# Optimization experiments

Hardware: AMD Instinct MI355X
Metric: run time of the kernel (lower is better)

The kernel has to match this reference:

```python
import jax, jax.numpy as jnp
import numpy as np

C = 128          # hidden_channels
H = 2            # num_heads
D = C // H       # head dim
L = 2            # HGTConv layers
T = 3            # node types: 0=paper, 1=author, 2=venue
N_NODES = [300000, 200000, 5000]
# edge types: (src_type_idx, dst_type_idx, n_edges)
EDGE_TYPES = [(1, 0, 150000), (0, 1, 150000), (0, 0, 120000),
              (0, 0, 120000), (0, 2, 30000), (2, 0, 30000)]
R = len(EDGE_TYPES)
N_LABEL = 200000
OFFS = np.concatenate([[0], np.cumsum(N_NODES)])  # global node offsets
N_TOT = int(OFFS[-1])


def setup_inputs() -> dict:
    key = jax.random.key(0)
    ks = iter(jax.random.split(key, 64))
    nrm = lambda shape: jax.random.normal(next(ks), shape, jnp.float32) * 0.05
    inp = {
        'paper_idx': jnp.arange(N_NODES[0]),
        'author_idx': jnp.arange(N_NODES[1]),
        'venue_idx': jnp.arange(N_NODES[2]),
    }
    for r, (s, d, e) in enumerate(EDGE_TYPES):
        inp[f'src{r}'] = jax.random.randint(next(ks), (e,), 0, N_NODES[s])
        inp[f'dst{r}'] = jax.random.randint(next(ks), (e,), 0, N_NODES[d])
    inp['edge_label_index'] = jax.random.randint(next(ks), (2, N_LABEL), 0, N_NODES[0])
    # learned parameters
    inp['paper_emb'] = nrm((N_NODES[0], C))
    inp['author_emb'] = nrm((N_NODES[1], C))
    inp['venue_emb'] = nrm((N_NODES[2], C))
    inp['lin_w'] = nrm((T, C, C));  inp['lin_b'] = nrm((T, C))           # HGT.lin_dict
    inp['kqv_w'] = nrm((L, T, C, 3 * C));  inp['kqv_b'] = nrm((L, T, 3 * C))
    inp['krel_w'] = nrm((L, R, H, D, D));  inp['vrel_w'] = nrm((L, R, H, D, D))
    inp['prel'] = jnp.ones((L, R, H), jnp.float32)                       # p_rel prior
    inp['out_w'] = nrm((L, T, C, C));  inp['out_b'] = nrm((L, T, C))     # out_lin
    inp['skip'] = jnp.ones((L, T), jnp.float32)                          # skip gate
    return inp


def _hgt_layer(xs, kqv_w, kqv_b, krel_w, vrel_w, prel, out_w, out_b, skip, srcs, dsts):
    # xs: list of [Nt, C] node features per node type
    k_d, q_d, v_d = [], [], []
    for t in range(T):
        kqv = xs[t] @ kqv_w[t] + kqv_b[t]                 # [Nt, 3C]
        k, q, v = jnp.split(kqv, 3, axis=1)
        k_d.append(k.reshape(-1, H, D))
        q_d.append(q.reshape(-1, H, D))
        v_d.append(v.reshape(-1, H, D))
    logits, vals, dstg = [], [], []
    scale = 1.0 / np.sqrt(D).astype(np.float32)
    for r, (s, d, _) in enumerate(EDGE_TYPES):
        # per-(edge_type, head) relation transforms on source k/v
        k_r = jnp.einsum('nhd,hde->nhe', k_d[s], krel_w[r])   # [Ns,H,D]
        v_r = jnp.einsum('nhd,hde->nhe', v_d[s], vrel_w[r])
        qe = q_d[d][dsts[r]]                                  # [E,H,D]
        ke = k_r[srcs[r]]
        logits.append((qe * ke).sum(-1) * prel[r] * scale)    # [E,H]
        vals.append(v_r[srcs[r]])                             # [E,H,D]
        dstg.append(dsts[r] + OFFS[d])
    logits = jnp.concatenate(logits)
    vals = jnp.concatenate(vals)
    dstg = jnp.concatenate(dstg)
    # softmax over all incoming edges per global destination node
    m = jax.ops.segment_max(logits, dstg, num_segments=N_TOT)
    e = jnp.exp(logits - m[dstg])
    den = jax.ops.segment_sum(e, dstg, num_segments=N_TOT)
    alpha = e / den[dstg]                                     # [E,H]
    agg = jax.ops.segment_sum(vals * alpha[:, :, None], dstg, num_segments=N_TOT)
    agg = agg.reshape(N_TOT, C)
    new_xs = []
    for t in range(T):
        o = agg[int(OFFS[t]):int(OFFS[t]) + N_NODES[t]]
        o = jax.nn.gelu(o) @ out_w[t] + out_b[t]
        a = jax.nn.sigmoid(skip[t])
        new_xs.append(a * o + (1.0 - a) * xs[t])
    return new_xs


def _forward(paper_idx, author_idx, venue_idx, srcs, dsts, edge_label_index,
             paper_emb, author_emb, venue_emb, lin_w, lin_b, kqv_w, kqv_b,
             krel_w, vrel_w, prel, out_w, out_b, skip):
    xs = [paper_emb[paper_idx], author_emb[author_idx], venue_emb[venue_idx]]
    # HGT per-node-type input projection + relu
    xs = [jax.nn.relu(xs[t] @ lin_w[t] + lin_b[t]) for t in range(T)]
    for l in range(L):
        xs = _hgt_layer(xs, kqv_w[l], kqv_b[l], krel_w[l], vrel_w[l], prel[l],
                        out_w[l], out_b[l], skip[l], srcs, dsts)
    xp = xs[0]  # paper embeddings
    return (xp[edge_label_index[0]] * xp[edge_label_index[1]]).sum(-1)


def reference(paper_idx, author_idx, venue_idx,
              src0, dst0, src1, dst1, src2, dst2, src3, dst3, src4, dst4, src5, dst5,
              edge_label_index, paper_emb, author_emb, venue_emb, lin_w, lin_b,
              kqv_w, kqv_b, krel_w, vrel_w, prel, out_w, out_b, skip):
    srcs = [src0, src1, src2, src3, src4, src5]
    dsts = [dst0, dst1, dst2, dst3, dst4, dst5]
    return _forward(paper_idx, author_idx, venue_idx, srcs, dsts, edge_label_index,
                    paper_emb, author_emb, venue_emb, lin_w, lin_b, kqv_w, kqv_b,
                    krel_w, vrel_w, prel, out_w, out_b, skip)
```

## Files before the change

kernel.cpp:

```cpp
#include <hip/hip_runtime.h>
#include <math.h>

#define NTOT 505000
#define NEDG 600000
#define NLBL 200000
#define NPAD 505856
#define NBLK 494

typedef __attribute__((ext_vector_type(8))) short s16x8;
typedef __attribute__((ext_vector_type(4))) float f32x4;

struct Ptr6 { const int* p[6]; };

__device__ inline float bf2f(unsigned short h) {
  union { unsigned u; float f; } v; v.u = ((unsigned)h) << 16; return v.f;
}
__device__ inline unsigned short f2bf(float f) {
  union { float f; unsigned u; } v; v.f = f;
  unsigned r = v.u + 0x7FFFu + ((v.u >> 16) & 1u);
  return (unsigned short)(r >> 16);
}
__device__ inline float gelu_t(float x) {
  return 0.5f * x * (1.f + tanhf(0.7978845608028654f * (x + 0.044715f * x * x * x)));
}
__device__ inline int d_esrc(int r) { return r == 0 ? 1 : (r == 5 ? 2 : 0); }
__device__ inline int edge_rel(int t) {
  return (t < 150000) ? 0 : (t < 300000) ? 1 : (t < 420000) ? 2
       : (t < 540000) ? 3 : (t < 570000) ? 4 : 5;
}
__device__ inline int rel_eoff(int r) {
  return r == 0 ? 0 : r == 1 ? 150000 : r == 2 ? 300000
       : r == 3 ? 420000 : r == 4 ? 540000 : 570000;
}
__device__ inline int rel_soff(int r) { return r == 0 ? 300000 : (r == 5 ? 500000 : 0); }
__device__ inline int rel_doff(int r) { return r == 1 ? 300000 : (r == 4 ? 500000 : 0); }

__global__ __launch_bounds__(256) void prep_transpose_k(
    const float* __restrict__ lin_w, const float* __restrict__ kqv_w,
    const float* __restrict__ out_w,
    unsigned short* __restrict__ linT, unsigned short* __restrict__ qT,
    unsigned short* __restrict__ outT)
{
  int t = blockIdx.x * 256 + threadIdx.x;
  if (t < 49152) {
    int tt = t / 16384, rem = t % 16384, n = rem / 128, k = rem % 128;
    linT[t] = f2bf(lin_w[(size_t)(tt * 128 + k) * 128 + n]);
    return;
  }
  t -= 49152;
  if (t < 98304) {
    int lt = t / 16384, rem = t % 16384, n = rem / 128, k = rem % 128;
    qT[t] = f2bf(kqv_w[(size_t)(lt * 128 + k) * 384 + 128 + n]);
    return;
  }
  t -= 98304;
  if (t < 98304) {
    int lt = t / 16384, rem = t % 16384, n = rem / 128, k = rem % 128;
    outT[t] = f2bf(out_w[(size_t)(lt * 128 + k) * 128 + n]);
  }
}

__global__ __launch_bounds__(256) void prep_rel_k(
    const float* __restrict__ kqv_w, const float* __restrict__ kqv_b,
    const float* __restrict__ krel_w, const float* __restrict__ vrel_w,
    unsigned short* __restrict__ WKT, unsigned short* __restrict__ WVT,
    float* __restrict__ bkp, float* __restrict__ bvp)
{
  int t = blockIdx.x * 256 + threadIdx.x;
  if (t < 393216) {
    int kv = t / 196608; int u = t % 196608;
    int l = u / 98304; u %= 98304;
    int r = u / 16384; u %= 16384;
    int n = u / 128, k = u % 128;
    int h = n >> 6, e2 = n & 63;
    int s = d_esrc(r);
    const float* W = kqv_w + ((size_t)(l * 3 + s) * 128 + k) * 384 + (kv ? 256 : 0) + h * 64;
    const float* Rw = (kv ? vrel_w : krel_w) + ((size_t)((l * 6 + r) * 2 + h) * 64) * 64 + e2;
    float sum = 0.f;
    for (int dd = 0; dd < 64; ++dd) sum += W[dd] * Rw[(size_t)dd * 64];
    (kv ? WVT : WKT)[((size_t)(l * 6 + r) * 128 + n) * 128 + k] = f2bf(sum);
    return;
  }
  t -= 393216;
  if (t < 3072) {
    int kv = t / 1536; int u = t % 1536;
    int l = u / 768; int rem = u % 768;
    int r = rem / 128, n = rem % 128;
    int h = n >> 6, e2 = n & 63;
    int s = d_esrc(r);
    const float* bb = kqv_b + (size_t)(l * 3 + s) * 384 + (kv ? 256 : 0) + h * 64;
    const float* Rw = (kv ? vrel_w : krel_w) + ((size_t)((l * 6 + r) * 2 + h) * 64) * 64 + e2;
    float sum = 0.f;
    for (int dd = 0; dd < 64; ++dd) sum += bb[dd] * Rw[(size_t)dd * 64];
    (kv ? bvp : bkp)[(l * 6 + r) * 128 + n] = sum;
  }
}

__global__ __launch_bounds__(256) void hist_k(Ptr6 dsts, unsigned* __restrict__ counts) {
  int t = blockIdx.x * 256 + threadIdx.x;
  if (t >= NEDG) return;
  int r = edge_rel(t);
  int e = t - rel_eoff(r);
  int gd = rel_doff(r) + dsts.p[r][e];
  atomicAdd(&counts[gd], 1u);
}

__global__ __launch_bounds__(256) void scanA_k(
    const unsigned* __restrict__ counts, unsigned* __restrict__ offs,
    unsigned* __restrict__ bsum)
{
  __shared__ unsigned sh[256];
  int b = blockIdx.x, tid = threadIdx.x;
  int base = b * 1024 + tid * 4;
  unsigned c0 = counts[base], c1 = counts[base + 1], c2 = counts[base + 2], c3 = counts[base + 3];
  unsigned s = c0 + c1 + c2 + c3;
  sh[tid] = s; __syncthreads();
  for (int o = 1; o < 256; o <<= 1) {
    unsigned v = (tid >= o) ? sh[tid - o] : 0u;
    __syncthreads();
    sh[tid] += v;
    __syncthreads();
  }
  unsigned texcl = sh[tid] - s;
  offs[base] = texcl;
  offs[base + 1] = texcl + c0;
  offs[base + 2] = texcl + c0 + c1;
  offs[base + 3] = texcl + c0 + c1 + c2;
  if (tid == 255) bsum[b] = sh[255];
}

__global__ __launch_bounds__(512) void scanB_k(
    const unsigned* __restrict__ bsum, unsigned* __restrict__ bpre,
    unsigned* __restrict__ offs)
{
  __shared__ unsigned sh[512];
  int tid = threadIdx.x;
  unsigned v = (tid < NBLK) ? bsum[tid] : 0u;
  sh[tid] = v; __syncthreads();
  for (int o = 1; o < 512; o <<= 1) {
    unsigned x = (tid >= o) ? sh[tid - o] : 0u;
    __syncthreads();
    sh[tid] += x;
    __syncthreads();
  }
  if (tid < NBLK) bpre[tid] = sh[tid] - v;
  if (tid == 511) offs[NTOT] = sh[511];
}

__global__ __launch_bounds__(256) void scanC_k(
    unsigned* __restrict__ offs, unsigned* __restrict__ cursor,
    const unsigned* __restrict__ bpre)
{
  int i = blockIdx.x * 256 + threadIdx.x;
  if (i >= NTOT) return;
  unsigned v = offs[i] + bpre[i >> 10];
  offs[i] = v;
  cursor[i] = v;
}

__global__ __launch_bounds__(256) void fill_k(
    Ptr6 srcs, Ptr6 dsts, unsigned* __restrict__ cursor,
    unsigned* __restrict__ lsrc, unsigned* __restrict__ leid)
{
  int t = blockIdx.x * 256 + threadIdx.x;
  if (t >= NEDG) return;
  int r = edge_rel(t);
  int e = t - rel_eoff(r);
  int gd = rel_doff(r) + dsts.p[r][e];
  int gs = rel_soff(r) + srcs.p[r][e];
  unsigned pos = atomicAdd(&cursor[gd], 1u);
  lsrc[pos] = ((unsigned)r << 24) | (unsigned)gs;
  leid[pos] = (unsigned)t;
}

template<int AF32, int GATHER, int ACT>
__global__ __launch_bounds__(256) void gemm_k(
    const void* __restrict__ Ap, const int* __restrict__ gidx,
    const unsigned short* __restrict__ BT, const float* __restrict__ bias,
    unsigned short* __restrict__ Y, int M)
{
  const int tid = threadIdx.x;
  const int wave = tid >> 6;
  const int lane = tid & 63;
  const int lrow = lane & 15;
  const int lgrp = lane >> 4;
  const int m0 = blockIdx.x * 64 + wave * 16;
  int arow = m0 + lrow;
  if (arow >= M) arow = M - 1;
  if (GATHER) arow = gidx[arow];
  f32x4 acc[8];
#pragma unroll
  for (int i = 0; i < 8; ++i) acc[i] = f32x4{0.f, 0.f, 0.f, 0.f};
#pragma unroll
  for (int ks = 0; ks < 4; ++ks) {
    const int k = ks * 32 + lgrp * 8;
    s16x8 a;
    if (AF32) {
      const float* pA = (const float*)Ap + (size_t)arow * 128 + k;
#pragma unroll
      for (int i = 0; i < 8; ++i) a[i] = (short)f2bf(pA[i]);
    } else {
      a = *(const s16x8*)((const unsigned short*)Ap + (size_t)arow * 128 + k);
    }
#pragma unroll
    for (int nf = 0; nf < 8; ++nf) {
      s16x8 b = *(const s16x8*)(BT + (size_t)(nf * 16 + lrow) * 128 + k);
      acc[nf] = __builtin_amdgcn_mfma_f32_16x16x32_bf16(a, b, acc[nf], 0, 0, 0);
    }
  }
#pragma unroll
  for (int nf = 0; nf < 8; ++nf) {
    const int col = nf * 16 + lrow;
    const float bv = bias[col];
#pragma unroll
    for (int r2 = 0; r2 < 4; ++r2) {
      const int row = m0 + lgrp * 4 + r2;
      if (row < M) {
        float v = acc[nf][r2] + bv;
        if (ACT == 1) v = v > 0.f ? v : 0.f;
        Y[(size_t)row * 128 + col] = f2bf(v);
      }
    }
  }
}

__global__ __launch_bounds__(256) void out_gemm_k(
    const unsigned short* __restrict__ AGG,
    const unsigned short* __restrict__ BT, const float* __restrict__ bias,
    const float* __restrict__ skipp,
    unsigned short* __restrict__ Xio, int M)
{
  const int tid = threadIdx.x;
  const int wave = tid >> 6;
  const int lane = tid & 63;
  const int lrow = lane & 15;
  const int lgrp = lane >> 4;
  const int m0 = blockIdx.x * 64 + wave * 16;
  int arow = m0 + lrow;
  if (arow >= M) arow = M - 1;
  f32x4 acc[8];
#pragma unroll
  for (int i = 0; i < 8; ++i) acc[i] = f32x4{0.f, 0.f, 0.f, 0.f};
#pragma unroll
  for (int ks = 0; ks < 4; ++ks) {
    const int k = ks * 32 + lgrp * 8;
    s16x8 raw = *(const s16x8*)(AGG + (size_t)arow * 128 + k);
    s16x8 a;
#pragma unroll
    for (int i = 0; i < 8; ++i)
      a[i] = (short)f2bf(gelu_t(bf2f((unsigned short)raw[i])));
#pragma unroll
    for (int nf = 0; nf < 8; ++nf) {
      s16x8 b = *(const s16x8*)(BT + (size_t)(nf * 16 + lrow) * 128 + k);
      acc[nf] = __builtin_amdgcn_mfma_f32_16x16x32_bf16(a, b, acc[nf], 0, 0, 0);
    }
  }
  const float sk = skipp[0];
  const float aa = 1.f / (1.f + expf(-sk));
#pragma unroll
  for (int nf = 0; nf < 8; ++nf) {
    const int col = nf * 16 + lrow;
    const float bv = bias[col];
#pragma unroll
    for (int r2 = 0; r2 < 4; ++r2) {
      const int row = m0 + lgrp * 4 + r2;
      if (row < M) {
        size_t idx = (size_t)row * 128 + col;
        float o = acc[nf][r2] + bv;
        float xo = bf2f(Xio[idx]);
        Xio[idx] = f2bf(aa * o + (1.f - aa) * xo);
      }
    }
  }
}

__global__ __launch_bounds__(256) void logit_k(
    const unsigned short* __restrict__ KR, const unsigned short* __restrict__ Q,
    const int* __restrict__ src, const int* __restrict__ dst,
    const float* __restrict__ prel2, float* __restrict__ logits,
    int nE, int dOff)
{
  int t = blockIdx.x * 256 + threadIdx.x;
  if (t >= nE * 2) return;
  int e = t >> 1, h = t & 1;
  int s = src[e];
  size_t g = (size_t)dOff + dst[e];
  const unsigned short* kp = KR + (size_t)s * 128 + h * 64;
  const unsigned short* qp = Q + g * 128 + h * 64;
  float sum = 0.f;
#pragma unroll
  for (int i = 0; i < 64; i += 8) {
    s16x8 kv = *(const s16x8*)(kp + i);
    s16x8 qv = *(const s16x8*)(qp + i);
#pragma unroll
    for (int j = 0; j < 8; ++j)
      sum += bf2f((unsigned short)kv[j]) * bf2f((unsigned short)qv[j]);
  }
  logits[(size_t)e * 2 + h] = sum * prel2[h] * 0.125f;
}

__global__ __launch_bounds__(256) void maxden_k(
    const unsigned* __restrict__ offs, const unsigned* __restrict__ leid,
    const float* __restrict__ logits, float* __restrict__ m_arr,
    float* __restrict__ invden)
{
  int t = blockIdx.x * 256 + threadIdx.x;
  if (t >= NTOT * 2) return;
  int n = t >> 1, h = t & 1;
  unsigned beg = offs[n], end = offs[n + 1];
  if (beg == end) { m_arr[t] = 0.f; invden[t] = 0.f; return; }
  float m = -1e30f;
  for (unsigned i = beg; i < end; ++i)
    m = fmaxf(m, logits[(size_t)leid[i] * 2 + h]);
  float den = 0.f;
  for (unsigned i = beg; i < end; ++i)
    den += expf(logits[(size_t)leid[i] * 2 + h] - m);
  m_arr[t] = m;
  invden[t] = 1.f / den;
}

template<int INIT>
__global__ __launch_bounds__(256) void gather_k(
    const unsigned short* __restrict__ VR, const unsigned* __restrict__ offs,
    const unsigned* __restrict__ lsrc, const unsigned* __restrict__ leid,
    const float* __restrict__ logits, const float* __restrict__ m_arr,
    const float* __restrict__ invden, unsigned short* __restrict__ AGG,
    int rel, int sOff, int dOff, int ndst)
{
  int t = blockIdx.x * 256 + threadIdx.x;
  if (t >= ndst * 8) return;
  int n = t >> 3, ck = t & 7, h = ck >> 2;
  int gd = dOff + n;
  unsigned beg = offs[gd], end = offs[gd + 1];
  float acc[16];
#pragma unroll
  for (int j = 0; j < 16; ++j) acc[j] = 0.f;
  int cnt = 0;
  float mh = 0.f, idh = 0.f;
  if (beg < end) { mh = m_arr[gd * 2 + h]; idh = invden[gd * 2 + h]; }
  for (unsigned i = beg; i < end; ++i) {
    unsigned u = lsrc[i];
    if ((int)(u >> 24) != rel) continue;
    int srow = (int)(u & 0xFFFFFFu) - sOff;
    float w = expf(logits[(size_t)leid[i] * 2 + h] - mh) * idh;
    const unsigned short* vp = VR + (size_t)srow * 128 + ck * 16;
    s16x8 v0 = *(const s16x8*)vp;
    s16x8 v1 = *(const s16x8*)(vp + 8);
#pragma unroll
    for (int j = 0; j < 8; ++j) {
      acc[j]     += w * bf2f((unsigned short)v0[j]);
      acc[8 + j] += w * bf2f((unsigned short)v1[j]);
    }
    ++cnt;
  }
  unsigned short* ap = AGG + (size_t)gd * 128 + ck * 16;
  if (INIT) {
    s16x8 r0, r1;
#pragma unroll
    for (int j = 0; j < 8; ++j) {
      r0[j] = (short)f2bf(acc[j]);
      r1[j] = (short)f2bf(acc[8 + j]);
    }
    *(s16x8*)ap = r0;
    *(s16x8*)(ap + 8) = r1;
  } else if (cnt) {
    s16x8 o0 = *(const s16x8*)ap, o1 = *(const s16x8*)(ap + 8);
    s16x8 r0, r1;
#pragma unroll
    for (int j = 0; j < 8; ++j) {
      r0[j] = (short)f2bf(acc[j] + bf2f((unsigned short)o0[j]));
      r1[j] = (short)f2bf(acc[8 + j] + bf2f((unsigned short)o1[j]));
    }
    *(s16x8*)ap = r0;
    *(s16x8*)(ap + 8) = r1;
  }
}

__global__ __launch_bounds__(256) void dot_k(
    const unsigned short* __restrict__ X, const int* __restrict__ eli,
    float* __restrict__ out)
{
  int i = blockIdx.x * 256 + threadIdx.x;
  if (i >= NLBL) return;
  const unsigned short* a = X + (size_t)eli[i] * 128;
  const unsigned short* b = X + (size_t)eli[NLBL + i] * 128;
  float s = 0.f;
#pragma unroll
  for (int c = 0; c < 128; c += 8) {
    s16x8 av = *(const s16x8*)(a + c);
    s16x8 bv = *(const s16x8*)(b + c);
#pragma unroll
    for (int j = 0; j < 8; ++j)
      s += bf2f((unsigned short)av[j]) * bf2f((unsigned short)bv[j]);
  }
  out[i] = s;
}

__global__ __launch_bounds__(256) void sentinel_k(float* out, int n, float v) {
  int i = blockIdx.x * 256 + threadIdx.x;
  if (i < n) out[i] = v;
}

extern "C" void kernel_launch(void* const* d_in, const int* in_sizes, int n_in,
                              void* d_out, int out_size, void* d_ws, size_t ws_size,
                              hipStream_t stream)
{
  static const int NNODES[3] = {300000, 200000, 5000};
  static const int OFFS[4] = {0, 300000, 500000, 505000};
  static const int ESRC[6] = {1, 0, 0, 0, 0, 2};
  static const int EDST[6] = {0, 1, 0, 0, 2, 0};
  static const int ECNT[6] = {150000, 150000, 120000, 120000, 30000, 30000};
  static const int EOFF[6] = {0, 150000, 300000, 420000, 540000, 570000};
  static const int SOFF[6] = {300000, 0, 0, 0, 0, 500000};
  static const int DOFF[6] = {0, 300000, 0, 0, 500000, 0};
  static const int INITR[6] = {1, 1, 0, 0, 1, 0};

  const int* idxs[3] = {(const int*)d_in[0], (const int*)d_in[1], (const int*)d_in[2]};
  Ptr6 srcs, dsts;
  for (int r = 0; r < 6; ++r) {
    srcs.p[r] = (const int*)d_in[3 + 2 * r];
    dsts.p[r] = (const int*)d_in[4 + 2 * r];
  }
  const int* eli = (const int*)d_in[15];
  const float* embs[3] = {(const float*)d_in[16], (const float*)d_in[17], (const float*)d_in[18]};
  const float* lin_w = (const float*)d_in[19];
  const float* lin_b = (const float*)d_in[20];
  const float* kqv_w = (const float*)d_in[21];
  const float* kqv_b = (const float*)d_in[22];
  const float* krel_w = (const float*)d_in[23];
  const float* vrel_w = (const float*)d_in[24];
  const float* prel = (const float*)d_in[25];
  const float* out_w = (const float*)d_in[26];
  const float* out_b = (const float*)d_in[27];
  const float* skip = (const float*)d_in[28];

  char* base = (char*)d_ws;
  size_t off = 0;
  auto carve = [&](size_t bytes) -> char* {
    char* r = base + off;
    off = (off + bytes + 255) & ~(size_t)255;
    return r;
  };
  unsigned short* X   = (unsigned short*)carve((size_t)NTOT * 256);
  unsigned short* QAG = (unsigned short*)carve((size_t)NTOT * 256);
  unsigned short* KV  = (unsigned short*)carve((size_t)300000 * 256);
  float* logits  = (float*)carve((size_t)NEDG * 8);
  float* m_arr   = (float*)carve((size_t)NTOT * 8);
  float* invden  = (float*)carve((size_t)NTOT * 8);
  unsigned* cnt_cur = (unsigned*)carve((size_t)NPAD * 4);
  unsigned* offsets = (unsigned*)carve((size_t)(NPAD + 8) * 4);
  unsigned* bsum = (unsigned*)carve(NBLK * 4);
  unsigned* bpre = (unsigned*)carve(NBLK * 4);
  unsigned* lsrc = (unsigned*)carve((size_t)NEDG * 4);
  unsigned* leid = (unsigned*)carve((size_t)NEDG * 4);
  unsigned short* linT = (unsigned short*)carve(49152 * 2);
  unsigned short* qT   = (unsigned short*)carve(98304 * 2);
  unsigned short* outT = (unsigned short*)carve(98304 * 2);
  unsigned short* WKT  = (unsigned short*)carve(196608 * 2);
  unsigned short* WVT  = (unsigned short*)carve(196608 * 2);
  float* bkp = (float*)carve(1536 * 4);
  float* bvp = (float*)carve(1536 * 4);

  if (off > ws_size) {
    sentinel_k<<<(NLBL + 255) / 256, 256, 0, stream>>>(
        (float*)d_out, out_size, (float)(ws_size >> 20));
    return;
  }

  prep_transpose_k<<<960, 256, 0, stream>>>(lin_w, kqv_w, out_w, linT, qT, outT);
  prep_rel_k<<<(393216 + 3072 + 255) / 256, 256, 0, stream>>>(
      kqv_w, kqv_b, krel_w, vrel_w, WKT, WVT, bkp, bvp);

  hipMemsetAsync(cnt_cur, 0, (size_t)NPAD * 4, stream);
  hist_k<<<(NEDG + 255) / 256, 256, 0, stream>>>(dsts, cnt_cur);
  scanA_k<<<NBLK, 256, 0, stream>>>(cnt_cur, offsets, bsum);
  scanB_k<<<1, 512, 0, stream>>>(bsum, bpre, offsets);
  scanC_k<<<(NTOT + 255) / 256, 256, 0, stream>>>(offsets, cnt_cur, bpre);
  fill_k<<<(NEDG + 255) / 256, 256, 0, stream>>>(srcs, dsts, cnt_cur, lsrc, leid);

  for (int t = 0; t < 3; ++t) {
    gemm_k<1, 1, 1><<<(NNODES[t] + 63) / 64, 256, 0, stream>>>(
        embs[t], idxs[t], linT + t * 16384, lin_b + t * 128,
        X + (size_t)OFFS[t] * 128, NNODES[t]);
  }

  for (int l = 0; l < 2; ++l) {
    for (int t = 0; t < 3; ++t) {
      gemm_k<0, 0, 0><<<(NNODES[t] + 63) / 64, 256, 0, stream>>>(
          X + (size_t)OFFS[t] * 128, nullptr, qT + (l * 3 + t) * 16384,
          kqv_b + (size_t)(l * 3 + t) * 384 + 128,
          QAG + (size_t)OFFS[t] * 128, NNODES[t]);
    }
    for (int r = 0; r < 6; ++r) {
      int s = ESRC[r], M = NNODES[s];
      gemm_k<0, 0, 0><<<(M + 63) / 64, 256, 0, stream>>>(
          X + (size_t)OFFS[s] * 128, nullptr, WKT + (l * 6 + r) * 16384,
          bkp + (l * 6 + r) * 128, KV, M);
      logit_k<<<(ECNT[r] * 2 + 255) / 256, 256, 0, stream>>>(
          KV, QAG, srcs.p[r], dsts.p[r], prel + (l * 6 + r) * 2,
          logits + (size_t)EOFF[r] * 2, ECNT[r], OFFS[EDST[r]]);
    }
    maxden_k<<<(NTOT * 2 + 255) / 256, 256, 0, stream>>>(
        offsets, leid, logits, m_arr, invden);
    for (int r = 0; r < 6; ++r) {
      int s = ESRC[r], M = NNODES[s];
      int nd = NNODES[EDST[r]];
      gemm_k<0, 0, 0><<<(M + 63) / 64, 256, 0, stream>>>(
          X + (size_t)OFFS[s] * 128, nullptr, WVT + (l * 6 + r) * 16384,
          bvp + (l * 6 + r) * 128, KV, M);
      if (INITR[r])
        gather_k<1><<<(nd * 8 + 255) / 256, 256, 0, stream>>>(
            KV, offsets, lsrc, leid, logits, m_arr, invden, QAG,
            r, SOFF[r], DOFF[r], nd);
      else
        gather_k<0><<<(nd * 8 + 255) / 256, 256, 0, stream>>>(
            KV, offsets, lsrc, leid, logits, m_arr, invden, QAG,
            r, SOFF[r], DOFF[r], nd);
    }
    for (int t = 0; t < 3; ++t) {
      out_gemm_k<<<(NNODES[t] + 63) / 64, 256, 0, stream>>>(
          QAG + (size_t)OFFS[t] * 128, outT + (l * 3 + t) * 16384,
          out_b + (l * 3 + t) * 128, skip + l * 3 + t,
          X + (size_t)OFFS[t] * 128, NNODES[t]);
    }
  }
  dot_k<<<(NLBL + 255) / 256, 256, 0, stream>>>(X, eli, (float*)d_out);
}
```

Baseline: 4.309 ms.

## Stage GEMM tiles in LDS, drop softmax max pass, write logits in CSR order

Result: faster. 3.772 ms (-12.5%).

```diff
diff --git a/kernel.cpp b/kernel.cpp
--- a/kernel.cpp
+++ b/kernel.cpp
@@ -160,7 +160,7 @@
 
 __global__ __launch_bounds__(256) void fill_k(
     Ptr6 srcs, Ptr6 dsts, unsigned* __restrict__ cursor,
-    unsigned* __restrict__ lsrc, unsigned* __restrict__ leid)
+    unsigned* __restrict__ lsrc, unsigned* __restrict__ einv)
 {
   int t = blockIdx.x * 256 + threadIdx.x;
   if (t >= NEDG) return;
@@ -170,106 +170,111 @@
   int gs = rel_soff(r) + srcs.p[r][e];
   unsigned pos = atomicAdd(&cursor[gd], 1u);
   lsrc[pos] = ((unsigned)r << 24) | (unsigned)gs;
-  leid[pos] = (unsigned)t;
-}
-
-template<int AF32, int GATHER, int ACT>
-__global__ __launch_bounds__(256) void gemm_k(
+  einv[t] = pos;
+}
+
+template<int MODE>
+__global__ __launch_bounds__(256) void gemm2_k(
     const void* __restrict__ Ap, const int* __restrict__ gidx,
     const unsigned short* __restrict__ BT, const float* __restrict__ bias,
-    unsigned short* __restrict__ Y, int M)
-{
+    const float* __restrict__ skipp, unsigned short* __restrict__ Y,
+    const unsigned short* __restrict__ Xio, int M)
+{
+  __shared__ unsigned short As[16384];
   const int tid = threadIdx.x;
+  const int blk = blockIdx.x;
+
+#pragma unroll
+  for (int j = 0; j < 8; ++j) {
+    int r = (tid >> 4) + j * 16;
+    int c = tid & 15;
+    int rg = blk * 128 + r;
+    if (rg >= M) rg = M - 1;
+    int slot = c ^ (r & 7);
+    s16x8 v;
+    if (MODE == 1) {
+      int grow = gidx[rg];
+      const float* pf = (const float*)Ap + (size_t)grow * 128 + c * 8;
+      f32x4 f0 = *(const f32x4*)pf;
+      f32x4 f1 = *(const f32x4*)(pf + 4);
+#pragma unroll
+      for (int i = 0; i < 4; ++i) v[i] = (short)f2bf(f0[i]);
+#pragma unroll
+      for (int i = 0; i < 4; ++i) v[4 + i] = (short)f2bf(f1[i]);
+    } else if (MODE == 2) {
+      s16x8 raw = *(const s16x8*)((const unsigned short*)Ap + (size_t)rg * 128 + c * 8);
+#pragma unroll
+      for (int i = 0; i < 8; ++i)
+        v[i] = (short)f2bf(gelu_t(bf2f((unsigned short)raw[i])));
+    } else {
+      v = *(const s16x8*)((const unsigned short*)Ap + (size_t)rg * 128 + c * 8);
+    }
+    *(s16x8*)(As + r * 128 + slot * 8) = v;
+  }
+  __syncthreads();
+
   const int wave = tid >> 6;
   const int lane = tid & 63;
   const int lrow = lane & 15;
   const int lgrp = lane >> 4;
-  const int m0 = blockIdx.x * 64 + wave * 16;
-  int arow = m0 + lrow;
-  if (arow >= M) arow = M - 1;
-  if (GATHER) arow = gidx[arow];
-  f32x4 acc[8];
-#pragma unroll
-  for (int i = 0; i < 8; ++i) acc[i] = f32x4{0.f, 0.f, 0.f, 0.f};
+  f32x4 acc[2][8];
+#pragma unroll
+  for (int rb = 0; rb < 2; ++rb)
+#pragma unroll
+    for (int nf = 0; nf < 8; ++nf) acc[rb][nf] = f32x4{0.f, 0.f, 0.f, 0.f};
+
 #pragma unroll
   for (int ks = 0; ks < 4; ++ks) {
-    const int k = ks * 32 + lgrp * 8;
-    s16x8 a;
-    if (AF32) {
-      const float* pA = (const float*)Ap + (size_t)arow * 128 + k;
-#pragma unroll
-      for (int i = 0; i < 8; ++i) a[i] = (short)f2bf(pA[i]);
-    } else {
-      a = *(const s16x8*)((const unsigned short*)Ap + (size_t)arow * 128 + k);
-    }
+    const int cA = ks * 4 + lgrp;
+    const int r0 = wave * 32 + lrow;
+    const int r1 = r0 + 16;
+    s16x8 a0 = *(const s16x8*)(As + r0 * 128 + ((cA ^ (r0 & 7)) << 3));
+    s16x8 a1 = *(const s16x8*)(As + r1 * 128 + ((cA ^ (r1 & 7)) << 3));
 #pragma unroll
     for (int nf = 0; nf < 8; ++nf) {
-      s16x8 b = *(const s16x8*)(BT + (size_t)(nf * 16 + lrow) * 128 + k);
-      acc[nf] = __builtin_amdgcn_mfma_f32_16x16x32_bf16(a, b, acc[nf], 0, 0, 0);
-    }
-  }
-#pragma unroll
-  for (int nf = 0; nf < 8; ++nf) {
-    const int col = nf * 16 + lrow;
-    const float bv = bias[col];
-#pragma unroll
-    for (int r2 = 0; r2 < 4; ++r2) {
-      const int row = m0 + lgrp * 4 + r2;
-      if (row < M) {
-        float v = acc[nf][r2] + bv;
-        if (ACT == 1) v = v > 0.f ? v : 0.f;
-        Y[(size_t)row * 128 + col] = f2bf(v);
+      s16x8 b = *(const s16x8*)(BT + (size_t)(nf * 16 + lrow) * 128 + ks * 32 + lgrp * 8);
+      acc[0][nf] = __builtin_amdgcn_mfma_f32_16x16x32_bf16(a0, b, acc[0][nf], 0, 0, 0);
+      acc[1][nf] = __builtin_amdgcn_mfma_f32_16x16x32_bf16(a1, b, acc[1][nf], 0, 0, 0);
+    }
+  }
+
+  __syncthreads();
+#pragma unroll
+  for (int rb = 0; rb < 2; ++rb) {
+#pragma unroll
+    for (int nf = 0; nf < 8; ++nf) {
+      const int col = nf * 16 + lrow;
+      const float bv = bias[col];
+#pragma unroll
+      for (int r2 = 0; r2 < 4; ++r2) {
+        const int row = wave * 32 + rb * 16 + lgrp * 4 + r2;
+        float v = acc[rb][nf][r2] + bv;
+        if (MODE == 1) v = v > 0.f ? v : 0.f;
+        As[row * 128 + ((((col >> 3) ^ (row & 7)) << 3) | (col & 7))] = f2bf(v);
       }
     }
   }
-}
-
-__global__ __launch_bounds__(256) void out_gemm_k(
-    const unsigned short* __restrict__ AGG,
-    const unsigned short* __restrict__ BT, const float* __restrict__ bias,
-    const float* __restrict__ skipp,
-    unsigned short* __restrict__ Xio, int M)
-{
-  const int tid = threadIdx.x;
-  const int wave = tid >> 6;
-  const int lane = tid & 63;
-  const int lrow = lane & 15;
-  const int lgrp = lane >> 4;
-  const int m0 = blockIdx.x * 64 + wave * 16;
-  int arow = m0 + lrow;
-  if (arow >= M) arow = M - 1;
-  f32x4 acc[8];
-#pragma unroll
-  for (int i = 0; i < 8; ++i) acc[i] = f32x4{0.f, 0.f, 0.f, 0.f};
-#pragma unroll
-  for (int ks = 0; ks < 4; ++ks) {
-    const int k = ks * 32 + lgrp * 8;
-    s16x8 raw = *(const s16x8*)(AGG + (size_t)arow * 128 + k);
-    s16x8 a;
-#pragma unroll
-    for (int i = 0; i < 8; ++i)
-      a[i] = (short)f2bf(gelu_t(bf2f((unsigned short)raw[i])));
-#pragma unroll
-    for (int nf = 0; nf < 8; ++nf) {
-      s16x8 b = *(const s16x8*)(BT + (size_t)(nf * 16 + lrow) * 128 + k);
-      acc[nf] = __builtin_amdgcn_mfma_f32_16x16x32_bf16(a, b, acc[nf], 0, 0, 0);
-    }
-  }
-  const float sk = skipp[0];
-  const float aa = 1.f / (1.f + expf(-sk));
-#pragma unroll
-  for (int nf = 0; nf < 8; ++nf) {
-    const int col = nf * 16 + lrow;
-    const float bv = bias[col];
-#pragma unroll
-    for (int r2 = 0; r2 < 4; ++r2) {
-      const int row = m0 + lgrp * 4 + r2;
-      if (row < M) {
-        size_t idx = (size_t)row * 128 + col;
-        float o = acc[nf][r2] + bv;
-        float xo = bf2f(Xio[idx]);
-        Xio[idx] = f2bf(aa * o + (1.f - aa) * xo);
+  __syncthreads();
+
+  float aa = 0.f;
+  if (MODE == 2) { float sk = skipp[0]; aa = 1.f / (1.f + expf(-sk)); }
+#pragma unroll
+  for (int j = 0; j < 8; ++j) {
+    int r = (tid >> 4) + j * 16;
+    int c = tid & 15;
+    int rg = blk * 128 + r;
+    if (rg < M) {
+      s16x8 v = *(const s16x8*)(As + r * 128 + ((c ^ (r & 7)) << 3));
+      if (MODE == 2) {
+        s16x8 xv = *(const s16x8*)(Xio + (size_t)rg * 128 + c * 8);
+        s16x8 o;
+#pragma unroll
+        for (int i = 0; i < 8; ++i)
+          o[i] = (short)f2bf(aa * bf2f((unsigned short)v[i]) +
+                             (1.f - aa) * bf2f((unsigned short)xv[i]));
+        v = o;
       }
+      *(s16x8*)(Y + (size_t)rg * 128 + c * 8) = v;
     }
   }
 }
@@ -277,8 +282,8 @@
 __global__ __launch_bounds__(256) void logit_k(
     const unsigned short* __restrict__ KR, const unsigned short* __restrict__ Q,
     const int* __restrict__ src, const int* __restrict__ dst,
-    const float* __restrict__ prel2, float* __restrict__ logits,
-    int nE, int dOff)
+    const float* __restrict__ prel2, const unsigned* __restrict__ einv,
+    float* __restrict__ logitsC, float* __restrict__ den, int nE, int dOff)
 {
   int t = blockIdx.x * 256 + threadIdx.x;
   if (t >= nE * 2) return;
@@ -296,83 +301,71 @@
     for (int j = 0; j < 8; ++j)
       sum += bf2f((unsigned short)kv[j]) * bf2f((unsigned short)qv[j]);
   }
-  logits[(size_t)e * 2 + h] = sum * prel2[h] * 0.125f;
-}
-
-__global__ __launch_bounds__(256) void maxden_k(
-    const unsigned* __restrict__ offs, const unsigned* __restrict__ leid,
-    const float* __restrict__ logits, float* __restrict__ m_arr,
-    float* __restrict__ invden)
+  float lg = sum * prel2[h] * 0.125f;
+  unsigned p = einv[e];
+  logitsC[(size_t)p * 2 + h] = lg;
+  atomicAdd(den + g * 2 + h, expf(lg));
+}
+
+__global__ __launch_bounds__(256) void invden_k(
+    const float* __restrict__ den, float* __restrict__ invden)
 {
   int t = blockIdx.x * 256 + threadIdx.x;
   if (t >= NTOT * 2) return;
-  int n = t >> 1, h = t & 1;
-  unsigned beg = offs[n], end = offs[n + 1];
-  if (beg == end) { m_arr[t] = 0.f; invden[t] = 0.f; return; }
-  float m = -1e30f;
-  for (unsigned i = beg; i < end; ++i)
-    m = fmaxf(m, logits[(size_t)leid[i] * 2 + h]);
-  float den = 0.f;
-  for (unsigned i = beg; i < end; ++i)
-    den += expf(logits[(size_t)leid[i] * 2 + h] - m);
-  m_arr[t] = m;
-  invden[t] = 1.f / den;
+  float d = den[t];
+  invden[t] = d > 0.f ? 1.f / d : 0.f;
 }
 
 template<int INIT>
 __global__ __launch_bounds__(256) void gather_k(
     const unsigned short* __restrict__ VR, const unsigned* __restrict__ offs,
-    const unsigned* __restrict__ lsrc, const unsigned* __restrict__ leid,
-    const float* __restrict__ logits, const float* __restrict__ m_arr,
+    const unsigned* __restrict__ lsrc, const float* __restrict__ logitsC,
     const float* __restrict__ invden, unsigned short* __restrict__ AGG,
     int rel, int sOff, int dOff, int ndst)
 {
   int t = blockIdx.x * 256 + threadIdx.x;
-  if (t >= ndst * 8) return;
-  int n = t >> 3, ck = t & 7, h = ck >> 2;
+  if (t >= ndst * 4) return;
+  int n = t >> 2, ck = t & 3, h = ck >> 1;
   int gd = dOff + n;
   unsigned beg = offs[gd], end = offs[gd + 1];
-  float acc[16];
-#pragma unroll
-  for (int j = 0; j < 16; ++j) acc[j] = 0.f;
+  float acc[32];
+#pragma unroll
+  for (int j = 0; j < 32; ++j) acc[j] = 0.f;
   int cnt = 0;
-  float mh = 0.f, idh = 0.f;
-  if (beg < end) { mh = m_arr[gd * 2 + h]; idh = invden[gd * 2 + h]; }
+  float idh = (beg < end) ? invden[gd * 2 + h] : 0.f;
   for (unsigned i = beg; i < end; ++i) {
     unsigned u = lsrc[i];
     if ((int)(u >> 24) != rel) continue;
     int srow = (int)(u & 0xFFFFFFu) - sOff;
-    float w = expf(logits[(size_t)leid[i] * 2 + h] - mh) * idh;
-    const unsigned short* vp = VR + (size_t)srow * 128 + ck * 16;
-    s16x8 v0 = *(const s16x8*)vp;
-    s16x8 v1 = *(const s16x8*)(vp + 8);
-#pragma unroll
-    for (int j = 0; j < 8; ++j) {
-      acc[j]     += w * bf2f((unsigned short)v0[j]);
-      acc[8 + j] += w * bf2f((unsigned short)v1[j]);
+    float w = expf(logitsC[(size_t)i * 2 + h]) * idh;
+    const unsigned short* vp = VR + (size_t)srow * 128 + ck * 32;
+#pragma unroll
+    for (int q = 0; q < 4; ++q) {
+      s16x8 vv = *(const s16x8*)(vp + q * 8);
+#pragma unroll
+      for (int j = 0; j < 8; ++j) acc[q * 8 + j] += w * bf2f((unsigned short)vv[j]);
     }
     ++cnt;
   }
-  unsigned short* ap = AGG + (size_t)gd * 128 + ck * 16;
+  unsigned short* ap = AGG + (size_t)gd * 128 + ck * 32;
   if (INIT) {
-    s16x8 r0, r1;
-#pragma unroll
-    for (int j = 0; j < 8; ++j) {
-      r0[j] = (short)f2bf(acc[j]);
-      r1[j] = (short)f2bf(acc[8 + j]);
-    }
-    *(s16x8*)ap = r0;
-    *(s16x8*)(ap + 8) = r1;
+#pragma unroll
+    for (int q = 0; q < 4; ++q) {
+      s16x8 r0;
+#pragma unroll
+      for (int j = 0; j < 8; ++j) r0[j] = (short)f2bf(acc[q * 8 + j]);
+      *(s16x8*)(ap + q * 8) = r0;
+    }
   } else if (cnt) {
-    s16x8 o0 = *(const s16x8*)ap, o1 = *(const s16x8*)(ap + 8);
-    s16x8 r0, r1;
-#pragma unroll
-    for (int j = 0; j < 8; ++j) {
-      r0[j] = (short)f2bf(acc[j] + bf2f((unsigned short)o0[j]));
-      r1[j] = (short)f2bf(acc[8 + j] + bf2f((unsigned short)o1[j]));
-    }
-    *(s16x8*)ap = r0;
-    *(s16x8*)(ap + 8) = r1;
+#pragma unroll
+    for (int q = 0; q < 4; ++q) {
+      s16x8 o0 = *(const s16x8*)(ap + q * 8);
+      s16x8 r0;
+#pragma unroll
+      for (int j = 0; j < 8; ++j)
+        r0[j] = (short)f2bf(acc[q * 8 + j] + bf2f((unsigned short)o0[j]));
+      *(s16x8*)(ap + q * 8) = r0;
+    }
   }
 }
 
@@ -444,15 +437,15 @@
   unsigned short* X   = (unsigned short*)carve((size_t)NTOT * 256);
   unsigned short* QAG = (unsigned short*)carve((size_t)NTOT * 256);
   unsigned short* KV  = (unsigned short*)carve((size_t)300000 * 256);
-  float* logits  = (float*)carve((size_t)NEDG * 8);
-  float* m_arr   = (float*)carve((size_t)NTOT * 8);
+  float* logitsC = (float*)carve((size_t)NEDG * 8);
+  float* den     = (float*)carve((size_t)NTOT * 8);
   float* invden  = (float*)carve((size_t)NTOT * 8);
   unsigned* cnt_cur = (unsigned*)carve((size_t)NPAD * 4);
   unsigned* offsets = (unsigned*)carve((size_t)(NPAD + 8) * 4);
   unsigned* bsum = (unsigned*)carve(NBLK * 4);
   unsigned* bpre = (unsigned*)carve(NBLK * 4);
   unsigned* lsrc = (unsigned*)carve((size_t)NEDG * 4);
-  unsigned* leid = (unsigned*)carve((size_t)NEDG * 4);
+  unsigned* einv = (unsigned*)carve((size_t)NEDG * 4);
   unsigned short* linT = (unsigned short*)carve(49152 * 2);
   unsigned short* qT   = (unsigned short*)carve(98304 * 2);
   unsigned short* outT = (unsigned short*)carve(98304 * 2);
@@ -476,52 +469,50 @@
   scanA_k<<<NBLK, 256, 0, stream>>>(cnt_cur, offsets, bsum);
   scanB_k<<<1, 512, 0, stream>>>(bsum, bpre, offsets);
   scanC_k<<<(NTOT + 255) / 256, 256, 0, stream>>>(offsets, cnt_cur, bpre);
-  fill_k<<<(NEDG + 255) / 256, 256, 0, stream>>>(srcs, dsts, cnt_cur, lsrc, leid);
+  fill_k<<<(NEDG + 255) / 256, 256, 0, stream>>>(srcs, dsts, cnt_cur, lsrc, einv);
 
   for (int t = 0; t < 3; ++t) {
-    gemm_k<1, 1, 1><<<(NNODES[t] + 63) / 64, 256, 0, stream>>>(
-        embs[t], idxs[t], linT + t * 16384, lin_b + t * 128,
-        X + (size_t)OFFS[t] * 128, NNODES[t]);
+    gemm2_k<1><<<(NNODES[t] + 127) / 128, 256, 0, stream>>>(
+        embs[t], idxs[t], linT + t * 16384, lin_b + t * 128, nullptr,
+        X + (size_t)OFFS[t] * 128, nullptr, NNODES[t]);
   }
 
   for (int l = 0; l < 2; ++l) {
+    hipMemsetAsync(den, 0, (size_t)NTOT * 8, stream);
     for (int t = 0; t < 3; ++t) {
-      gemm_k<0, 0, 0><<<(NNODES[t] + 63) / 64, 256, 0, stream>>>(
+      gemm2_k<0><<<(NNODES[t] + 127) / 128, 256, 0, stream>>>(
           X + (size_t)OFFS[t] * 128, nullptr, qT + (l * 3 + t) * 16384,
-          kqv_b + (size_t)(l * 3 + t) * 384 + 128,
-          QAG + (size_t)OFFS[t] * 128, NNODES[t]);
+          kqv_b + (size_t)(l * 3 + t) * 384 + 128, nullptr,
+          QAG + (size_t)OFFS[t] * 128, nullptr, NNODES[t]);
     }
     for (int r = 0; r < 6; ++r) {
       int s = ESRC[r], M = NNODES[s];
-      gemm_k<0, 0, 0><<<(M + 63) / 64, 256, 0, stream>>>(
+      gemm2_k<0><<<(M + 127) / 128, 256, 0, stream>>>(
           X + (size_t)OFFS[s] * 128, nullptr, WKT + (l * 6 + r) * 16384,
-          bkp + (l * 6 + r) * 128, KV, M);
+          bkp + (l * 6 + r) * 128, nullptr, KV, nullptr, M);
       logit_k<<<(ECNT[r] * 2 + 255) / 256, 256, 0, stream>>>(
           KV, QAG, srcs.p[r], dsts.p[r], prel + (l * 6 + r) * 2,
-          logits + (size_t)EOFF[r] * 2, ECNT[r], OFFS[EDST[r]]);
-    }
-    maxden_k<<<(NTOT * 2 + 255) / 256, 256, 0, stream>>>(
-        offsets, leid, logits, m_arr, invden);
+          einv + EOFF[r], logitsC, den, ECNT[r], OFFS[EDST[r]]);
+    }
+    invden_k<<<(NTOT * 2 + 255) / 256, 256, 0, stream>>>(den, invden);
     for (int r = 0; r < 6; ++r) {
       int s = ESRC[r], M = NNODES[s];
       int nd = NNODES[EDST[r]];
-      gemm_k<0, 0, 0><<<(M + 63) / 64, 256, 0, stream>>>(
+      gemm2_k<0><<<(M + 127) / 128, 256, 0, stream>>>(
           X + (size_t)OFFS[s] * 128, nullptr, WVT + (l * 6 + r) * 16384,
-          bvp + (l * 6 + r) * 128, KV, M);
+          bvp + (l * 6 + r) * 128, nullptr, KV, nullptr, M);
       if (INITR[r])
-        gather_k<1><<<(nd * 8 + 255) / 256, 256, 0, stream>>>(
-            KV, offsets, lsrc, leid, logits, m_arr, invden, QAG,
-            r, SOFF[r], DOFF[r], nd);
+        gather_k<1><<<(nd * 4 + 255) / 256, 256, 0, stream>>>(
+            KV, offsets, lsrc, logitsC, invden, QAG, r, SOFF[r], DOFF[r], nd);
       else
-        gather_k<0><<<(nd * 8 + 255) / 256, 256, 0, stream>>>(
-            KV, offsets, lsrc, leid, logits, m_arr, invden, QAG,
-            r, SOFF[r], DOFF[r], nd);
+        gather_k<0><<<(nd * 4 + 255) / 256, 256, 0, stream>>>(
+            KV, offsets, lsrc, logitsC, invden, QAG, r, SOFF[r], DOFF[r], nd);
     }
     for (int t = 0; t < 3; ++t) {
-      out_gemm_k<<<(NNODES[t] + 63) / 64, 256, 0, stream>>>(
-          QAG + (size_t)OFFS[t] * 128, outT + (l * 3 + t) * 16384,
+      gemm2_k<2><<<(NNODES[t] + 127) / 128, 256, 0, stream>>>(
+          QAG + (size_t)OFFS[t] * 128, nullptr, outT + (l * 3 + t) * 16384,
           out_b + (l * 3 + t) * 128, skip + l * 3 + t,
-          X + (size_t)OFFS[t] * 128, NNODES[t]);
+          X + (size_t)OFFS[t] * 128, X + (size_t)OFFS[t] * 128, NNODES[t]);
     }
   }
   dot_k<<<(NLBL + 255) / 256, 256, 0, stream>>>(X, eli, (float*)d_out);
```
